# Optimization experiments

Measured on AMD Instinct MI355X. Metric: run time of the kernel, lower is better.

Reference implementation:

```python
import jax, jax.numpy as jnp
import numpy as np

COMMITMENT_COST = 0.25


def setup_inputs() -> dict:
    key = jax.random.key(0)
    k1, k2 = jax.random.split(key)
    z = jax.random.normal(k1, (16, 64, 64, 64), dtype=jnp.float32)  # [B, C=embed_dim, H, W]
    embedding = jax.random.normal(k2, (1024, 64), dtype=jnp.float32)  # [K, D]
    return {"z": z, "embedding": embedding}


def reference(z, embedding):
    B, C, H, W = z.shape
    K, D = embedding.shape
    # NCHW -> NHWC, flatten to [N, D]
    z_perm = jnp.transpose(z, (0, 2, 3, 1))
    z_flat = z_perm.reshape(-1, D)
    N = z_flat.shape[0]
    # squared L2 distances: ||z||^2 + ||e||^2 - 2 z e^T  -> [N, K]
    distances = (
        jnp.sum(z_flat ** 2, axis=1, keepdims=True)
        + jnp.sum(embedding ** 2, axis=1)
        - 2.0 * jnp.matmul(z_flat, embedding.T)
    )
    encoding_indices = jnp.argmin(distances, axis=1)  # [N]
    # gather instead of one-hot matmul (same math, efficient)
    quantized = embedding[encoding_indices].reshape(z_perm.shape)
    # commitment loss (eval-mode forward; EMA buffer updates are train-only side effects)
    e_latent_loss = jnp.mean((jax.lax.stop_gradient(quantized) - z_perm) ** 2)
    loss = COMMITMENT_COST * e_latent_loss
    # straight-through estimator
    quantized_st = z_perm + jax.lax.stop_gradient(quantized - z_perm)
    quantized_out = jnp.transpose(quantized_st, (0, 3, 1, 2))
    # perplexity from code usage histogram (== mean of one-hot encodings)
    avg_probs = jnp.zeros((K,), dtype=jnp.float32).at[encoding_indices].add(1.0) / N
    perplexity = jnp.exp(-jnp.sum(avg_probs * jnp.log(avg_probs + 1e-10)))
    return quantized_out, loss, encoding_indices.reshape(B, H, W), perplexity
```

## Files before the change

### kernel.cpp

```cpp
#include <hip/hip_runtime.h>
#include <math.h>


#define QOUT_SZ  4194304
#define LOSS_OFF QOUT_SZ
#define IDX_OFF  (QOUT_SZ + 1)
#define PERP_OFF (QOUT_SZ + 1 + 65536)

typedef _Float16 f16x8 __attribute__((ext_vector_type(8)));
typedef _Float16 f16x4 __attribute__((ext_vector_type(4)));
typedef float    f32x4 __attribute__((ext_vector_type(4)));

#define WS_EHI   0
#define WS_ELO   131072
#define WS_ESQ   262144
#define WS_HIST  266240
#define WS_LOSS  270336

__device__ __forceinline__ void gll16(const void* g, void* l) {
    __builtin_amdgcn_global_load_lds(
        (const __attribute__((address_space(1))) void*)g,
        (__attribute__((address_space(3))) void*)l, 16, 0, 0);
}

__global__ void vq_pre(const float* __restrict__ emb,
                       _Float16* __restrict__ ehi, _Float16* __restrict__ elo,
                       float* __restrict__ esq, float* __restrict__ hist) {
    const int t = threadIdx.x;
    const int g = blockIdx.x * 256 + t;
    float4 v = ((const float4*)emb)[g];
    float xs[4] = {v.x, v.y, v.z, v.w};
    f16x4 hi, lo;
    float ss = 0.f;
#pragma unroll
    for (int j = 0; j < 4; ++j) {
        _Float16 h = (_Float16)xs[j];
        hi[j] = h;
        lo[j] = (_Float16)((xs[j] - (float)h) * 4096.0f);
        ss = fmaf(xs[j], xs[j], ss);
    }
    ((f16x4*)ehi)[g] = hi;
    ((f16x4*)elo)[g] = lo;
    ss += __shfl_xor(ss, 1, 64);
    ss += __shfl_xor(ss, 2, 64);
    ss += __shfl_xor(ss, 4, 64);
    ss += __shfl_xor(ss, 8, 64);
    if ((t & 15) == 0) esq[g >> 4] = -0.5f * ss;
    if (blockIdx.x < 4) hist[blockIdx.x * 256 + t] = 0.f;
}

__launch_bounds__(256, 4)
__global__ void vq_main(const float* __restrict__ z,
                        const float* __restrict__ emb,
                        const _Float16* __restrict__ gehi,
                        const _Float16* __restrict__ gelo,
                        const float* __restrict__ gesq,
                        float* __restrict__ hist,
                        float* __restrict__ lossp,
                        float* __restrict__ out) {
    __shared__ __align__(16) char es[32768];
    __shared__ float esql[1024];
    __shared__ float candv[128];
    __shared__ int   candi[128];
    __shared__ int   idxs[64];
    __shared__ float redw[4];

    const int tid  = threadIdx.x;
    const int blk  = blockIdx.x;
    const int b    = blk >> 6;
    const int h    = blk & 63;
    const int lane = tid & 63;
    const int wv   = tid >> 6;
    const int pg   = wv & 1;
    const int ksel = wv >> 1;
    const int col  = lane & 15;
    const int g    = lane >> 4;

#pragma unroll
    for (int i = 0; i < 4; ++i) esql[tid + 256 * i] = gesq[tid + 256 * i];

    const float* zb = z + (size_t)b * 262144 + (size_t)h * 64;
    const float* zrow = zb + pg * 32 + col;
    f16x8 Ah[2][2], Al[2][2];
#pragma unroll
    for (int pt = 0; pt < 2; ++pt) {
#pragma unroll
        for (int m = 0; m < 2; ++m) {
#pragma unroll
            for (int j = 0; j < 8; ++j) {
                int c = m * 32 + g * 8 + j;
                float x = zrow[pt * 16 + (size_t)c * 4096];
                _Float16 hh = (_Float16)x;
                Ah[pt][m][j] = hh;
                Al[pt][m][j] = (_Float16)((x - (float)hh) * 4096.0f);
            }
        }
    }

    const char* gh = (const char*)gehi;
    const char* gl = (const char*)gelo;
    const int u0 = tid, u1 = tid + 256;
    const int c0 = u0 >> 3, c1 = u1 >> 3;
    const size_t so0 = (size_t)c0 * 128 + (size_t)(((u0 & 7) ^ (c0 & 7)) * 16);
    const size_t so1 = (size_t)c1 * 128 + (size_t)(((u1 & 7) ^ (c1 & 7)) * 16);
    char* const dA = es + wv * 1024;

#define STAGE(n, bb) do { \
        const size_t gb_ = (size_t)(n) * 8192; \
        char* d_ = dA + (bb) * 16384; \
        gll16(gh + gb_ + so0, d_);            \
        gll16(gh + gb_ + so1, d_ + 4096);     \
        gll16(gl + gb_ + so0, d_ + 8192);     \
        gll16(gl + gb_ + so1, d_ + 12288);    \
    } while (0)

    int rb[2][2];
#pragma unroll
    for (int ct = 0; ct < 2; ++ct) {
        int cl = ksel * 32 + ct * 16 + col;
#pragma unroll
        for (int m = 0; m < 2; ++m)
            rb[ct][m] = cl * 128 + ((((m * 4 + g) * 16)) ^ ((col & 7) << 4));
    }

    float best[2][4];
    int   besti[2][4];
#pragma unroll
    for (int pt = 0; pt < 2; ++pt)
#pragma unroll
        for (int r = 0; r < 4; ++r) { best[pt][r] = -3.4e38f; besti[pt][r] = 0; }

    STAGE(0, 0);

    for (int sc = 0; sc < 16; ++sc) {
        const int cur = sc & 1;
        asm volatile("s_waitcnt vmcnt(0)" ::: "memory");
        __builtin_amdgcn_s_barrier();
        asm volatile("" ::: "memory");
        if (sc < 15) STAGE(sc + 1, cur ^ 1);

        const char* bp = es + cur * 16384;
        const int kb = sc * 64 + ksel * 32;
#pragma unroll
        for (int ct = 0; ct < 2; ++ct) {
            const float e2  = esql[kb + ct * 16 + col];
            const int  kidx = kb + ct * 16 + col;
            f16x8 Bh0 = *(const f16x8*)(bp + rb[ct][0]);
            f16x8 Bh1 = *(const f16x8*)(bp + rb[ct][1]);
            f16x8 Bl0 = *(const f16x8*)(bp + 8192 + rb[ct][0]);
            f16x8 Bl1 = *(const f16x8*)(bp + 8192 + rb[ct][1]);
#pragma unroll
            for (int pt = 0; pt < 2; ++pt) {
                f32x4 ah = {e2, e2, e2, e2};
                f32x4 ax = {0.f, 0.f, 0.f, 0.f};
                ah = __builtin_amdgcn_mfma_f32_16x16x32_f16(Ah[pt][0], Bh0, ah, 0, 0, 0);
                ah = __builtin_amdgcn_mfma_f32_16x16x32_f16(Ah[pt][1], Bh1, ah, 0, 0, 0);
                ax = __builtin_amdgcn_mfma_f32_16x16x32_f16(Ah[pt][0], Bl0, ax, 0, 0, 0);
                ax = __builtin_amdgcn_mfma_f32_16x16x32_f16(Ah[pt][1], Bl1, ax, 0, 0, 0);
                ax = __builtin_amdgcn_mfma_f32_16x16x32_f16(Al[pt][0], Bh0, ax, 0, 0, 0);
                ax = __builtin_amdgcn_mfma_f32_16x16x32_f16(Al[pt][1], Bh1, ax, 0, 0, 0);
#pragma unroll
                for (int r = 0; r < 4; ++r) {
                    float mval = fmaf(0x1p-12f, ax[r], ah[r]);
                    if (mval > best[pt][r]) { best[pt][r] = mval; besti[pt][r] = kidx; }
                }
            }
        }
    }
#undef STAGE

#pragma unroll
    for (int mask = 1; mask <= 8; mask <<= 1) {
#pragma unroll
        for (int pt = 0; pt < 2; ++pt)
#pragma unroll
            for (int r = 0; r < 4; ++r) {
                float ov = __shfl_xor(best[pt][r], mask, 64);
                int   oi = __shfl_xor(besti[pt][r], mask, 64);
                if (ov > best[pt][r] ||
                    (ov == best[pt][r] && oi < besti[pt][r])) {
                    best[pt][r] = ov; besti[pt][r] = oi;
                }
            }
    }
    if (col == 0) {
#pragma unroll
        for (int pt = 0; pt < 2; ++pt)
#pragma unroll
            for (int r = 0; r < 4; ++r) {
                int p = pg * 32 + pt * 16 + g * 4 + r;
                candv[p * 2 + ksel] = best[pt][r];
                candi[p * 2 + ksel] = besti[pt][r];
            }
    }
    __syncthreads();

    if (tid < 64) {
        float v0 = candv[tid * 2],     v1 = candv[tid * 2 + 1];
        int   i0 = candi[tid * 2],     i1 = candi[tid * 2 + 1];
        int bi = (v1 > v0 || (v1 == v0 && i1 < i0)) ? i1 : i0;
        idxs[tid] = bi;
        atomicAdd(&hist[bi], 1.0f);
        out[(size_t)IDX_OFF + blk * 64 + tid] = (float)bi;
    }
    __syncthreads();

    const int w  = tid & 63;
    const int cq = tid >> 6;
    const int idx = idxs[w];
    const float* ev = emb + (size_t)idx * 64 + cq * 16;
    const float* zr = zb + w;
    float* outq = out + (size_t)b * 262144 + (size_t)h * 64 + w;
    float lsum = 0.f;
#pragma unroll
    for (int i = 0; i < 4; ++i) {
        float4 qv = *(const float4*)(ev + i * 4);
        float q4[4] = {qv.x, qv.y, qv.z, qv.w};
#pragma unroll
        for (int jj = 0; jj < 4; ++jj) {
            int c = cq * 16 + i * 4 + jj;
            float zv = zr[(size_t)c * 4096];
            outq[(size_t)c * 4096] = q4[jj];
            float d = q4[jj] - zv;
            lsum = fmaf(d, d, lsum);
        }
    }
#pragma unroll
    for (int off = 32; off > 0; off >>= 1)
        lsum += __shfl_xor(lsum, off, 64);
    if (lane == 0) redw[wv] = lsum;
    __syncthreads();
    if (tid == 0)
        lossp[blk] = redw[0] + redw[1] + redw[2] + redw[3];
}

__global__ void vq_fin(const float* __restrict__ hist,
                       const float* __restrict__ lossp,
                       float* __restrict__ out) {
    __shared__ float sh[1024];
    __shared__ float sl[1024];
    int t = threadIdx.x;
    float hc = hist[t];
    float p  = hc * (1.0f / 65536.0f);
    sh[t] = p * logf(p + 1e-10f);
    sl[t] = lossp[t];
    __syncthreads();
    for (int s = 512; s > 0; s >>= 1) {
        if (t < s) { sh[t] += sh[t + s]; sl[t] += sl[t + s]; }
        __syncthreads();
    }
    if (t == 0) {
        out[LOSS_OFF] = 0.25f * sl[0] / (float)QOUT_SZ;
        out[PERP_OFF] = expf(-sh[0]);
    }
}

extern "C" void kernel_launch(void* const* d_in, const int* in_sizes, int n_in,
                              void* d_out, int out_size, void* d_ws, size_t ws_size,
                              hipStream_t stream) {
    const float* z   = (const float*)d_in[0];
    const float* emb = (const float*)d_in[1];
    float* out = (float*)d_out;
    char*  ws  = (char*)d_ws;

    _Float16* ehi   = (_Float16*)(ws + WS_EHI);
    _Float16* elo   = (_Float16*)(ws + WS_ELO);
    float*    esq   = (float*)(ws + WS_ESQ);
    float*    hist  = (float*)(ws + WS_HIST);
    float*    lossp = (float*)(ws + WS_LOSS);

    vq_pre<<<64, 256, 0, stream>>>(emb, ehi, elo, esq, hist);
    vq_main<<<1024, 256, 0, stream>>>(z, emb, ehi, elo, esq, hist, lossp, out);
    vq_fin<<<1, 1024, 0, stream>>>(hist, lossp, out);
}
```

Before: 67.55 us.

## Halve block to two waves, each scanning all codes for its points

The main kernel now runs with 128 threads, and each wave covers all 64 codes of a chunk for its 32 pixels. Before, work was split across waves by code half and then merged through shared memory. This drops the cross-wave candidate merge and one barrier. It issues the first embedding stage before the z loads so they overlap, and splits the low-part accumulator into two independent MFMA chains. In exchange each wave does twice the MFMA work per chunk, and there are fewer waves per block to hide latency.

```diff
diff --git a/kernel.cpp b/kernel.cpp
--- a/kernel.cpp
+++ b/kernel.cpp
@@ -49,7 +49,7 @@
     if (blockIdx.x < 4) hist[blockIdx.x * 256 + t] = 0.f;
 }
 
-__launch_bounds__(256, 4)
+__launch_bounds__(128, 2)
 __global__ void vq_main(const float* __restrict__ z,
                         const float* __restrict__ emb,
                         const _Float16* __restrict__ gehi,
@@ -60,10 +60,8 @@
                         float* __restrict__ out) {
     __shared__ __align__(16) char es[32768];
     __shared__ float esql[1024];
-    __shared__ float candv[128];
-    __shared__ int   candi[128];
     __shared__ int   idxs[64];
-    __shared__ float redw[4];
+    __shared__ float redw[2];
 
     const int tid  = threadIdx.x;
     const int blk  = blockIdx.x;
@@ -71,16 +69,37 @@
     const int h    = blk & 63;
     const int lane = tid & 63;
     const int wv   = tid >> 6;
-    const int pg   = wv & 1;
-    const int ksel = wv >> 1;
     const int col  = lane & 15;
     const int g    = lane >> 4;
 
 #pragma unroll
-    for (int i = 0; i < 4; ++i) esql[tid + 256 * i] = gesq[tid + 256 * i];
+    for (int i = 0; i < 8; ++i) esql[tid + 128 * i] = gesq[tid + 128 * i];
+
+    const char* gh = (const char*)gehi;
+    const char* gl = (const char*)gelo;
+    size_t so[4];
+#pragma unroll
+    for (int i = 0; i < 4; ++i) {
+        int u = tid + 128 * i;
+        int c = u >> 3;
+        so[i] = (size_t)c * 128 + (size_t)(((u & 7) ^ (c & 7)) << 4);
+    }
+#define STAGE(n, bo) do {                                                 \
+        const size_t gb_ = (size_t)(n) * 8192;                            \
+        gll16(gh + gb_ + so[0], es + (bo) + 0 * 2048 + wv * 1024);        \
+        gll16(gh + gb_ + so[1], es + (bo) + 1 * 2048 + wv * 1024);        \
+        gll16(gh + gb_ + so[2], es + (bo) + 2 * 2048 + wv * 1024);        \
+        gll16(gh + gb_ + so[3], es + (bo) + 3 * 2048 + wv * 1024);        \
+        gll16(gl + gb_ + so[0], es + (bo) + 8192 + 0 * 2048 + wv * 1024); \
+        gll16(gl + gb_ + so[1], es + (bo) + 8192 + 1 * 2048 + wv * 1024); \
+        gll16(gl + gb_ + so[2], es + (bo) + 8192 + 2 * 2048 + wv * 1024); \
+        gll16(gl + gb_ + so[3], es + (bo) + 8192 + 3 * 2048 + wv * 1024); \
+    } while (0)
+
+    STAGE(0, 0);
 
     const float* zb = z + (size_t)b * 262144 + (size_t)h * 64;
-    const float* zrow = zb + pg * 32 + col;
+    const float* zrw = zb + wv * 32 + col;
     f16x8 Ah[2][2], Al[2][2];
 #pragma unroll
     for (int pt = 0; pt < 2; ++pt) {
@@ -89,7 +108,7 @@
 #pragma unroll
             for (int j = 0; j < 8; ++j) {
                 int c = m * 32 + g * 8 + j;
-                float x = zrow[pt * 16 + (size_t)c * 4096];
+                float x = zrw[pt * 16 + (size_t)c * 4096];
                 _Float16 hh = (_Float16)x;
                 Ah[pt][m][j] = hh;
                 Al[pt][m][j] = (_Float16)((x - (float)hh) * 4096.0f);
@@ -97,30 +116,13 @@
         }
     }
 
-    const char* gh = (const char*)gehi;
-    const char* gl = (const char*)gelo;
-    const int u0 = tid, u1 = tid + 256;
-    const int c0 = u0 >> 3, c1 = u1 >> 3;
-    const size_t so0 = (size_t)c0 * 128 + (size_t)(((u0 & 7) ^ (c0 & 7)) * 16);
-    const size_t so1 = (size_t)c1 * 128 + (size_t)(((u1 & 7) ^ (c1 & 7)) * 16);
-    char* const dA = es + wv * 1024;
-
-#define STAGE(n, bb) do { \
-        const size_t gb_ = (size_t)(n) * 8192; \
-        char* d_ = dA + (bb) * 16384; \
-        gll16(gh + gb_ + so0, d_);            \
-        gll16(gh + gb_ + so1, d_ + 4096);     \
-        gll16(gl + gb_ + so0, d_ + 8192);     \
-        gll16(gl + gb_ + so1, d_ + 12288);    \
-    } while (0)
-
-    int rb[2][2];
-#pragma unroll
-    for (int ct = 0; ct < 2; ++ct) {
-        int cl = ksel * 32 + ct * 16 + col;
+    int rb[4][2];
+#pragma unroll
+    for (int ct = 0; ct < 4; ++ct) {
+        int cl = ct * 16 + col;
 #pragma unroll
         for (int m = 0; m < 2; ++m)
-            rb[ct][m] = cl * 128 + ((((m * 4 + g) * 16)) ^ ((col & 7) << 4));
+            rb[ct][m] = cl * 128 + ((((m << 2) + g) ^ (col & 7)) << 4);
     }
 
     float best[2][4];
@@ -130,39 +132,38 @@
 #pragma unroll
         for (int r = 0; r < 4; ++r) { best[pt][r] = -3.4e38f; besti[pt][r] = 0; }
 
-    STAGE(0, 0);
-
     for (int sc = 0; sc < 16; ++sc) {
-        const int cur = sc & 1;
         asm volatile("s_waitcnt vmcnt(0)" ::: "memory");
         __builtin_amdgcn_s_barrier();
         asm volatile("" ::: "memory");
-        if (sc < 15) STAGE(sc + 1, cur ^ 1);
-
-        const char* bp = es + cur * 16384;
-        const int kb = sc * 64 + ksel * 32;
-#pragma unroll
-        for (int ct = 0; ct < 2; ++ct) {
-            const float e2  = esql[kb + ct * 16 + col];
-            const int  kidx = kb + ct * 16 + col;
+        const int bo = (sc & 1) * 16384;
+        if (sc < 15) STAGE(sc + 1, bo ^ 16384);
+
+        const char* bp = es + bo;
+        const int kb = sc * 64;
+#pragma unroll
+        for (int ct = 0; ct < 4; ++ct) {
+            const int  kcol = kb + ct * 16 + col;
+            const float e2  = esql[kcol];
             f16x8 Bh0 = *(const f16x8*)(bp + rb[ct][0]);
             f16x8 Bh1 = *(const f16x8*)(bp + rb[ct][1]);
             f16x8 Bl0 = *(const f16x8*)(bp + 8192 + rb[ct][0]);
             f16x8 Bl1 = *(const f16x8*)(bp + 8192 + rb[ct][1]);
 #pragma unroll
             for (int pt = 0; pt < 2; ++pt) {
-                f32x4 ah = {e2, e2, e2, e2};
-                f32x4 ax = {0.f, 0.f, 0.f, 0.f};
-                ah = __builtin_amdgcn_mfma_f32_16x16x32_f16(Ah[pt][0], Bh0, ah, 0, 0, 0);
-                ah = __builtin_amdgcn_mfma_f32_16x16x32_f16(Ah[pt][1], Bh1, ah, 0, 0, 0);
-                ax = __builtin_amdgcn_mfma_f32_16x16x32_f16(Ah[pt][0], Bl0, ax, 0, 0, 0);
-                ax = __builtin_amdgcn_mfma_f32_16x16x32_f16(Ah[pt][1], Bl1, ax, 0, 0, 0);
-                ax = __builtin_amdgcn_mfma_f32_16x16x32_f16(Al[pt][0], Bh0, ax, 0, 0, 0);
-                ax = __builtin_amdgcn_mfma_f32_16x16x32_f16(Al[pt][1], Bh1, ax, 0, 0, 0);
+                f32x4 ah  = {e2, e2, e2, e2};
+                f32x4 ax1 = {0.f, 0.f, 0.f, 0.f};
+                f32x4 ax2 = {0.f, 0.f, 0.f, 0.f};
+                ah  = __builtin_amdgcn_mfma_f32_16x16x32_f16(Ah[pt][0], Bh0, ah,  0, 0, 0);
+                ah  = __builtin_amdgcn_mfma_f32_16x16x32_f16(Ah[pt][1], Bh1, ah,  0, 0, 0);
+                ax1 = __builtin_amdgcn_mfma_f32_16x16x32_f16(Ah[pt][0], Bl0, ax1, 0, 0, 0);
+                ax1 = __builtin_amdgcn_mfma_f32_16x16x32_f16(Ah[pt][1], Bl1, ax1, 0, 0, 0);
+                ax2 = __builtin_amdgcn_mfma_f32_16x16x32_f16(Al[pt][0], Bh0, ax2, 0, 0, 0);
+                ax2 = __builtin_amdgcn_mfma_f32_16x16x32_f16(Al[pt][1], Bh1, ax2, 0, 0, 0);
 #pragma unroll
                 for (int r = 0; r < 4; ++r) {
-                    float mval = fmaf(0x1p-12f, ax[r], ah[r]);
-                    if (mval > best[pt][r]) { best[pt][r] = mval; besti[pt][r] = kidx; }
+                    float mval = fmaf(0x1p-12f, ax1[r] + ax2[r], ah[r]);
+                    if (mval > best[pt][r]) { best[pt][r] = mval; besti[pt][r] = kcol; }
                 }
             }
         }
@@ -187,38 +188,30 @@
 #pragma unroll
         for (int pt = 0; pt < 2; ++pt)
 #pragma unroll
-            for (int r = 0; r < 4; ++r) {
-                int p = pg * 32 + pt * 16 + g * 4 + r;
-                candv[p * 2 + ksel] = best[pt][r];
-                candi[p * 2 + ksel] = besti[pt][r];
-            }
+            for (int r = 0; r < 4; ++r)
+                idxs[wv * 32 + pt * 16 + g * 4 + r] = besti[pt][r];
     }
     __syncthreads();
 
     if (tid < 64) {
-        float v0 = candv[tid * 2],     v1 = candv[tid * 2 + 1];
-        int   i0 = candi[tid * 2],     i1 = candi[tid * 2 + 1];
-        int bi = (v1 > v0 || (v1 == v0 && i1 < i0)) ? i1 : i0;
-        idxs[tid] = bi;
+        int bi = idxs[tid];
         atomicAdd(&hist[bi], 1.0f);
         out[(size_t)IDX_OFF + blk * 64 + tid] = (float)bi;
     }
-    __syncthreads();
 
     const int w  = tid & 63;
-    const int cq = tid >> 6;
     const int idx = idxs[w];
-    const float* ev = emb + (size_t)idx * 64 + cq * 16;
+    const float* ev = emb + (size_t)idx * 64 + wv * 32;
     const float* zr = zb + w;
     float* outq = out + (size_t)b * 262144 + (size_t)h * 64 + w;
     float lsum = 0.f;
 #pragma unroll
-    for (int i = 0; i < 4; ++i) {
+    for (int i = 0; i < 8; ++i) {
         float4 qv = *(const float4*)(ev + i * 4);
         float q4[4] = {qv.x, qv.y, qv.z, qv.w};
 #pragma unroll
         for (int jj = 0; jj < 4; ++jj) {
-            int c = cq * 16 + i * 4 + jj;
+            int c = wv * 32 + i * 4 + jj;
             float zv = zr[(size_t)c * 4096];
             outq[(size_t)c * 4096] = q4[jj];
             float d = q4[jj] - zv;
@@ -231,7 +224,7 @@
     if (lane == 0) redw[wv] = lsum;
     __syncthreads();
     if (tid == 0)
-        lossp[blk] = redw[0] + redw[1] + redw[2] + redw[3];
+        lossp[blk] = redw[0] + redw[1];
 }
 
 __global__ void vq_fin(const float* __restrict__ hist,
@@ -270,6 +263,6 @@
     float*    lossp = (float*)(ws + WS_LOSS);
 
     vq_pre<<<64, 256, 0, stream>>>(emb, ehi, elo, esq, hist);
-    vq_main<<<1024, 256, 0, stream>>>(z, emb, ehi, elo, esq, hist, lossp, out);
+    vq_main<<<1024, 128, 0, stream>>>(z, emb, ehi, elo, esq, hist, lossp, out);
     vq_fin<<<1, 1024, 0, stream>>>(hist, lossp, out);
 }
```

After: 67.23 us. Within noise of the previous version (-0.5%).

## Stage only high-half codebook in LDS and read low half from global

Applied to the files above, without the earlier changes.

The LDS stage buffer now holds only the high-precision half of the codebook, covering 128 codes per stage instead of 64, so the loop runs 8 stages instead of 16 and needs half as many barriers. The low-precision correction half is read directly from global memory (expected to hit cache) with a small software prefetch interleaved across the four column tiles. This cuts LDS traffic and synchronisation, but puts global-load latency inside the MFMA loop. The s_waitcnt vmcnt(0) at each stage boundary now also waits on those direct loads.

```diff
diff --git a/kernel.cpp b/kernel.cpp
--- a/kernel.cpp
+++ b/kernel.cpp
@@ -99,28 +99,31 @@
 
     const char* gh = (const char*)gehi;
     const char* gl = (const char*)gelo;
-    const int u0 = tid, u1 = tid + 256;
-    const int c0 = u0 >> 3, c1 = u1 >> 3;
-    const size_t so0 = (size_t)c0 * 128 + (size_t)(((u0 & 7) ^ (c0 & 7)) * 16);
-    const size_t so1 = (size_t)c1 * 128 + (size_t)(((u1 & 7) ^ (c1 & 7)) * 16);
-    char* const dA = es + wv * 1024;
-
-#define STAGE(n, bb) do { \
-        const size_t gb_ = (size_t)(n) * 8192; \
-        char* d_ = dA + (bb) * 16384; \
-        gll16(gh + gb_ + so0, d_);            \
-        gll16(gh + gb_ + so1, d_ + 4096);     \
-        gll16(gl + gb_ + so0, d_ + 8192);     \
-        gll16(gl + gb_ + so1, d_ + 12288);    \
+    size_t so[4];
+#pragma unroll
+    for (int i = 0; i < 4; ++i) {
+        int u = tid + 256 * i;
+        int c = u >> 3;
+        so[i] = (size_t)c * 128 + (size_t)(((u & 7) ^ (c & 7)) << 4);
+    }
+
+#define STAGE(n, bb) do {                                                  \
+        const size_t gb_ = (size_t)(n) * 16384;                            \
+        gll16(gh + gb_ + so[0], es + (bb) + 0 * 4096 + wv * 1024);         \
+        gll16(gh + gb_ + so[1], es + (bb) + 1 * 4096 + wv * 1024);         \
+        gll16(gh + gb_ + so[2], es + (bb) + 2 * 4096 + wv * 1024);         \
+        gll16(gh + gb_ + so[3], es + (bb) + 3 * 4096 + wv * 1024);         \
     } while (0)
 
-    int rb[2][2];
-#pragma unroll
-    for (int ct = 0; ct < 2; ++ct) {
-        int cl = ksel * 32 + ct * 16 + col;
-#pragma unroll
-        for (int m = 0; m < 2; ++m)
-            rb[ct][m] = cl * 128 + ((((m * 4 + g) * 16)) ^ ((col & 7) << 4));
+    int rb[4][2], rblo[4][2];
+#pragma unroll
+    for (int ct = 0; ct < 4; ++ct) {
+        int cl = ksel * 64 + ct * 16 + col;
+#pragma unroll
+        for (int m = 0; m < 2; ++m) {
+            rb[ct][m]   = cl * 128 + ((((m << 2) + g) ^ (col & 7)) << 4);
+            rblo[ct][m] = cl * 128 + (((m << 2) + g) << 4);
+        }
     }
 
     float best[2][4];
@@ -132,41 +135,54 @@
 
     STAGE(0, 0);
 
-    for (int sc = 0; sc < 16; ++sc) {
+#define COMPUTE(ct, BL0, BL1) do {                                         \
+        const int  kidx = kb + (ct) * 16 + col;                            \
+        const float e2  = esql[kidx];                                      \
+        f16x8 Bh0 = *(const f16x8*)(bp + rb[ct][0]);                       \
+        f16x8 Bh1 = *(const f16x8*)(bp + rb[ct][1]);                       \
+        _Pragma("unroll")                                                   \
+        for (int pt = 0; pt < 2; ++pt) {                                    \
+            f32x4 ah = {e2, e2, e2, e2};                                    \
+            f32x4 ax = {0.f, 0.f, 0.f, 0.f};                                \
+            ah = __builtin_amdgcn_mfma_f32_16x16x32_f16(Ah[pt][0], Bh0, ah, 0, 0, 0); \
+            ah = __builtin_amdgcn_mfma_f32_16x16x32_f16(Ah[pt][1], Bh1, ah, 0, 0, 0); \
+            ax = __builtin_amdgcn_mfma_f32_16x16x32_f16(Ah[pt][0], BL0, ax, 0, 0, 0); \
+            ax = __builtin_amdgcn_mfma_f32_16x16x32_f16(Ah[pt][1], BL1, ax, 0, 0, 0); \
+            ax = __builtin_amdgcn_mfma_f32_16x16x32_f16(Al[pt][0], Bh0, ax, 0, 0, 0); \
+            ax = __builtin_amdgcn_mfma_f32_16x16x32_f16(Al[pt][1], Bh1, ax, 0, 0, 0); \
+            _Pragma("unroll")                                               \
+            for (int r = 0; r < 4; ++r) {                                   \
+                float mval = fmaf(0x1p-12f, ax[r], ah[r]);                  \
+                if (mval > best[pt][r]) { best[pt][r] = mval; besti[pt][r] = kidx; } \
+            }                                                               \
+        }                                                                   \
+    } while (0)
+
+    for (int sc = 0; sc < 8; ++sc) {
         const int cur = sc & 1;
         asm volatile("s_waitcnt vmcnt(0)" ::: "memory");
         __builtin_amdgcn_s_barrier();
         asm volatile("" ::: "memory");
-        if (sc < 15) STAGE(sc + 1, cur ^ 1);
-
-        const char* bp = es + cur * 16384;
-        const int kb = sc * 64 + ksel * 32;
-#pragma unroll
-        for (int ct = 0; ct < 2; ++ct) {
-            const float e2  = esql[kb + ct * 16 + col];
-            const int  kidx = kb + ct * 16 + col;
-            f16x8 Bh0 = *(const f16x8*)(bp + rb[ct][0]);
-            f16x8 Bh1 = *(const f16x8*)(bp + rb[ct][1]);
-            f16x8 Bl0 = *(const f16x8*)(bp + 8192 + rb[ct][0]);
-            f16x8 Bl1 = *(const f16x8*)(bp + 8192 + rb[ct][1]);
-#pragma unroll
-            for (int pt = 0; pt < 2; ++pt) {
-                f32x4 ah = {e2, e2, e2, e2};
-                f32x4 ax = {0.f, 0.f, 0.f, 0.f};
-                ah = __builtin_amdgcn_mfma_f32_16x16x32_f16(Ah[pt][0], Bh0, ah, 0, 0, 0);
-                ah = __builtin_amdgcn_mfma_f32_16x16x32_f16(Ah[pt][1], Bh1, ah, 0, 0, 0);
-                ax = __builtin_amdgcn_mfma_f32_16x16x32_f16(Ah[pt][0], Bl0, ax, 0, 0, 0);
-                ax = __builtin_amdgcn_mfma_f32_16x16x32_f16(Ah[pt][1], Bl1, ax, 0, 0, 0);
-                ax = __builtin_amdgcn_mfma_f32_16x16x32_f16(Al[pt][0], Bh0, ax, 0, 0, 0);
-                ax = __builtin_amdgcn_mfma_f32_16x16x32_f16(Al[pt][1], Bh1, ax, 0, 0, 0);
-#pragma unroll
-                for (int r = 0; r < 4; ++r) {
-                    float mval = fmaf(0x1p-12f, ax[r], ah[r]);
-                    if (mval > best[pt][r]) { best[pt][r] = mval; besti[pt][r] = kidx; }
-                }
-            }
-        }
-    }
+        if (sc < 7) STAGE(sc + 1, (cur ^ 1) * 16384);
+
+        const char* bp  = es + cur * 16384;
+        const char* glc = gl + (size_t)sc * 16384;
+        const int kb = sc * 128 + ksel * 64;
+
+        f16x8 La0 = *(const f16x8*)(glc + rblo[0][0]);
+        f16x8 La1 = *(const f16x8*)(glc + rblo[0][1]);
+        f16x8 Lb0 = *(const f16x8*)(glc + rblo[1][0]);
+        f16x8 Lb1 = *(const f16x8*)(glc + rblo[1][1]);
+        COMPUTE(0, La0, La1);
+        La0 = *(const f16x8*)(glc + rblo[2][0]);
+        La1 = *(const f16x8*)(glc + rblo[2][1]);
+        COMPUTE(1, Lb0, Lb1);
+        Lb0 = *(const f16x8*)(glc + rblo[3][0]);
+        Lb1 = *(const f16x8*)(glc + rblo[3][1]);
+        COMPUTE(2, La0, La1);
+        COMPUTE(3, Lb0, Lb1);
+    }
+#undef COMPUTE
 #undef STAGE
 
 #pragma unroll
```

After: 107.1 us. 58.6% more time.
